# Kernel optimization log

Measured on AMD Instinct MI355X. Metric: run time of the kernel, lower is better.

The kernel has to match this reference:

```python
import jax, jax.numpy as jnp
import numpy as np

N_PTS = 32768      # n_x == n_y (query points == source points)
K_NBR = 32         # neighbors per query point
N_EDGES = N_PTS * K_NBR
D_COORD = 3
C = 64             # f_y channels == MLP output channels
H = 256            # MLP hidden width


def setup_inputs() -> dict:
    key = jax.random.key(0)
    ks = jax.random.split(key, 12)
    y = jax.random.normal(ks[0], (N_PTS, D_COORD), dtype=jnp.float32)
    x = jax.random.normal(ks[1], (N_PTS, D_COORD), dtype=jnp.float32)
    f_y = jax.random.normal(ks[2], (N_PTS, C), dtype=jnp.float32)
    neighbors_index = jax.random.randint(ks[3], (N_EDGES,), 0, N_PTS, dtype=jnp.int64)
    neighbors_row_splits = (jnp.arange(N_PTS + 1, dtype=jnp.int64) * K_NBR)
    weights = jax.random.uniform(ks[4], (N_EDGES,), dtype=jnp.float32)
    # LinearChannelMLP params: layers [6, 256, 256, 64], gelu between layers
    def dense(k, fan_in, fan_out):
        w = jax.random.normal(k, (fan_in, fan_out), dtype=jnp.float32) / np.sqrt(fan_in)
        return w
    W0 = dense(ks[5], 2 * D_COORD, H)
    b0 = jnp.zeros((H,), dtype=jnp.float32)
    W1 = dense(ks[6], H, H)
    b1 = jnp.zeros((H,), dtype=jnp.float32)
    W2 = dense(ks[7], H, C)
    b2 = jnp.zeros((C,), dtype=jnp.float32)
    return {"y": y, "x": x, "f_y": f_y,
            "neighbors_index": neighbors_index,
            "neighbors_row_splits": neighbors_row_splits,
            "weights": weights,
            "W0": W0, "b0": b0, "W1": W1, "b1": b1, "W2": W2, "b2": b2}


def reference(y, x, f_y, neighbors_index, neighbors_row_splits, weights,
              W0, b0, W1, b1, W2, b2):
    n_x = neighbors_row_splits.shape[0] - 1
    n_edges = neighbors_index.shape[0]
    # CSR row id for each edge (equivalent to repeat(arange(n_x), num_reps))
    seg = jnp.searchsorted(neighbors_row_splits, jnp.arange(n_edges), side='right') - 1
    rep_features = y[neighbors_index]            # [E, 3] gathered source coords
    self_features = x[seg]                       # [E, 3] repeated query coords
    agg = jnp.concatenate([rep_features, self_features], axis=-1)  # [E, 6]
    # channel MLP (gelu between layers, none after last)
    h = jax.nn.gelu(agg @ W0 + b0)
    h = jax.nn.gelu(h @ W1 + b1)
    rep = h @ W2 + b2                            # [E, C] kernel values
    # transform_type='linear': kernel * f_y(neighbor)
    rep = rep * f_y[neighbors_index]
    # quadrature weights (forces sum reduction, as in source)
    rep = rep * weights[:, None]
    out = jax.ops.segment_sum(rep, seg, num_segments=n_x)  # segment-CSR sum
    return out
```

## Files before the change

### kernel.cpp

```cpp
#include <hip/hip_runtime.h>
#include <hip/hip_bf16.h>
#include <stdint.h>

#define NPTS 32768
#define KNBR 32
#define NEDGES (NPTS * KNBR)
#define TM 128
#define AGG_STRIDE 40
#define H_STRIDE 264

typedef __attribute__((ext_vector_type(8))) short short8;
typedef __attribute__((ext_vector_type(4))) float f32x4;
typedef __attribute__((ext_vector_type(4))) unsigned int u32x4;
typedef __attribute__((ext_vector_type(2))) unsigned int u32x2;

__device__ __forceinline__ unsigned short f2bf(float f) {
    unsigned int u = __float_as_uint(f);
    unsigned int r = (u + 0x7FFFu + ((u >> 16) & 1u)) >> 16;
    return (unsigned short)r;
}

__device__ __forceinline__ unsigned int cvt_pk_bf16(float lo, float hi) {
    unsigned int r;
    asm("v_cvt_pk_bf16_f32 %0, %1, %2" : "=v"(r) : "v"(lo), "v"(hi));
    return r;
}

__device__ __forceinline__ float gelu_tanh(float x) {
    float x2 = x * x;
    float u = fmaf(-0.102942496f, x2, -2.30220824f);
    float e = __builtin_amdgcn_exp2f(x * u);
    return x * __builtin_amdgcn_rcpf(1.0f + e);
}

__global__ void pack_w(const float* __restrict__ W0, const float* __restrict__ W1,
                       const float* __restrict__ W2, unsigned short* __restrict__ wp) {
    int tid = blockIdx.x * blockDim.x + threadIdx.x;
    if (tid >= 176 * 64) return;
    int fid = tid >> 6, l = tid & 63, ln = l & 15, lg = l >> 4;
    unsigned short v[8];
    if (fid < 16) {
        int nt = fid, k0 = lg * 8;
        #pragma unroll
        for (int j = 0; j < 8; ++j) {
            int k = k0 + j;
            v[j] = f2bf(k < 6 ? W0[k * 256 + nt * 16 + ln] : 0.0f);
        }
    } else if (fid < 144) {
        int g = fid - 16;
        int nt = g >> 3, s = g & 7;
        int col = nt * 16 + ln;
        int k0 = s * 32 + lg * 8;
        #pragma unroll
        for (int j = 0; j < 8; ++j) v[j] = f2bf(W1[(k0 + j) * 256 + col]);
    } else {
        int g = fid - 144;
        int c = g >> 3, s = g & 7;
        int col = c * 16 + ln;
        int k0 = s * 32 + lg * 8;
        #pragma unroll
        for (int j = 0; j < 8; ++j) v[j] = f2bf(W2[(k0 + j) * 64 + col]);
    }
    unsigned short* o = &wp[tid * 8];
    #pragma unroll
    for (int j = 0; j < 8; ++j) o[j] = v[j];
}

__global__ __launch_bounds__(512, 4)
void gno_fused(const float* __restrict__ y, const float* __restrict__ x,
               const float* __restrict__ f_y, const int* __restrict__ nbr,
               const float* __restrict__ wts,
               const float* __restrict__ b0, const float* __restrict__ b1,
               const float* __restrict__ b2,
               const unsigned short* __restrict__ wp,
               float* __restrict__ out) {
    __shared__ __align__(16) unsigned short agg_lds[TM * AGG_STRIDE];
    __shared__ __align__(16) unsigned short h_lds[TM * H_STRIDE];

    const int b = blockIdx.x;
    const int tid = threadIdx.x;
    const int l = tid & 63;
    const int w = tid >> 6;
    const int wm = w & 1;
    const int wn = w >> 1;
    const int lg = l >> 4;
    const int ln = l & 15;
    const int ebase = b * TM;

    const char* wpb = (const char*)wp;
    const char* pW0 = wpb + wn * 4096 + l * 16;
    const char* pW1 = wpb + 16384 + wn * 32768 + l * 16;
    const char* pW2 = wpb + 147456 + wn * 8192 + l * 16;
    const char* aggb = (const char*)agg_lds + ln * 80 + lg * 16;
    char* hwb = (char*)h_lds + ln * 528 + wn * 128 + lg * 8;
    const char* hrb = (const char*)h_lds + ln * 528 + lg * 16;

    if (tid < TM) {
        int e = ebase + tid;
        int j = nbr[e];
        int i = e >> 5;
        const float* yr = &y[j * 3];
        const float* xr = &x[i * 3];
        u32x4 q0;
        q0.x = cvt_pk_bf16(yr[0], yr[1]);
        q0.y = cvt_pk_bf16(yr[2], xr[0]);
        q0.z = cvt_pk_bf16(xr[1], xr[2]);
        q0.w = 0u;
        u32x4 z = {0u, 0u, 0u, 0u};
        unsigned short* row = &agg_lds[tid * AGG_STRIDE];
        *(u32x4*)(row +  0) = q0;
        *(u32x4*)(row +  8) = z;
        *(u32x4*)(row + 16) = z;
        *(u32x4*)(row + 24) = z;
    }
    __syncthreads();

    {
        short8 ag[4];
        #pragma unroll
        for (int mt = 0; mt < 4; ++mt)
            ag[mt] = *(const short8*)(aggb + (4 * wm + mt) * 1280);
        #pragma unroll
        for (int q = 0; q < 4; ++q) {
            short8 aw = *(const short8*)(pW0 + q * 1024);
            f32x4 b0f = *(const f32x4*)&b0[(4 * wn + q) * 16 + lg * 4];
            #pragma unroll
            for (int mt = 0; mt < 4; ++mt) {
                f32x4 c = __builtin_amdgcn_mfma_f32_16x16x32_bf16(aw, ag[mt], b0f, 0, 0, 0);
                u32x2 pv;
                pv.x = cvt_pk_bf16(gelu_tanh(c[0]), gelu_tanh(c[1]));
                pv.y = cvt_pk_bf16(gelu_tanh(c[2]), gelu_tanh(c[3]));
                *(u32x2*)(hwb + (4 * wm + mt) * 8448 + q * 32) = pv;
            }
        }
    }
    __syncthreads();

    f32x4 acc[4][4];
    #pragma unroll
    for (int q = 0; q < 4; ++q) {
        f32x4 b1f = *(const f32x4*)&b1[(4 * wn + q) * 16 + lg * 4];
        #pragma unroll
        for (int mt = 0; mt < 4; ++mt) acc[mt][q] = b1f;
    }
    #pragma unroll
    for (int s = 0; s < 8; ++s) {
        short8 hb[4];
        #pragma unroll
        for (int mt = 0; mt < 4; ++mt)
            hb[mt] = *(const short8*)(hrb + (4 * wm + mt) * 8448 + s * 64);
        #pragma unroll
        for (int q = 0; q < 4; ++q) {
            short8 aw = *(const short8*)(pW1 + q * 8192 + s * 1024);
            #pragma unroll
            for (int mt = 0; mt < 4; ++mt)
                acc[mt][q] = __builtin_amdgcn_mfma_f32_16x16x32_bf16(aw, hb[mt], acc[mt][q], 0, 0, 0);
        }
    }
    __syncthreads();

    #pragma unroll
    for (int q = 0; q < 4; ++q) {
        #pragma unroll
        for (int mt = 0; mt < 4; ++mt) {
            u32x2 pv;
            pv.x = cvt_pk_bf16(gelu_tanh(acc[mt][q][0]), gelu_tanh(acc[mt][q][1]));
            pv.y = cvt_pk_bf16(gelu_tanh(acc[mt][q][2]), gelu_tanh(acc[mt][q][3]));
            *(u32x2*)(hwb + (4 * wm + mt) * 8448 + q * 32) = pv;
        }
    }
    __syncthreads();

    f32x4 fy[4];
    float wv[4];
    #pragma unroll
    for (int m = 0; m < 4; ++m) {
        int e = ebase + (wm * 4 + m) * 16 + ln;
        int j = nbr[e];
        fy[m] = *(const f32x4*)&f_y[j * 64 + wn * 16 + lg * 4];
        wv[m] = wts[e];
    }

    f32x4 acc3[4];
    {
        f32x4 b2f = *(const f32x4*)&b2[wn * 16 + lg * 4];
        #pragma unroll
        for (int m = 0; m < 4; ++m) acc3[m] = b2f;
    }
    const char* hrb3 = hrb + wm * 33792;
    #pragma unroll
    for (int s = 0; s < 8; ++s) {
        short8 aw = *(const short8*)(pW2 + s * 1024);
        #pragma unroll
        for (int m = 0; m < 4; ++m) {
            short8 hb = *(const short8*)(hrb3 + m * 8448 + s * 64);
            acc3[m] = __builtin_amdgcn_mfma_f32_16x16x32_bf16(aw, hb, acc3[m], 0, 0, 0);
        }
    }

    {
        f32x4 seg[2];
        seg[0] = (f32x4){0.f, 0.f, 0.f, 0.f};
        seg[1] = (f32x4){0.f, 0.f, 0.f, 0.f};
        #pragma unroll
        for (int m = 0; m < 4; ++m) {
            f32x4 v;
            #pragma unroll
            for (int i = 0; i < 4; ++i)
                v[i] = acc3[m][i] * fy[m][i] * wv[m];
            seg[m >> 1] += v;
        }
        #pragma unroll
        for (int g = 0; g < 2; ++g) {
            f32x4 v = seg[g];
            #pragma unroll
            for (int d = 1; d <= 8; d <<= 1) {
                #pragma unroll
                for (int i = 0; i < 4; ++i)
                    v[i] += __shfl_xor(v[i], d, 64);
            }
            if (ln == 0)
                *(f32x4*)&out[(b * 4 + wm * 2 + g) * 64 + wn * 16 + lg * 4] = v;
        }
    }
}

extern "C" void kernel_launch(void* const* d_in, const int* in_sizes, int n_in,
                              void* d_out, int out_size, void* d_ws, size_t ws_size,
                              hipStream_t stream) {
    const float* y   = (const float*)d_in[0];
    const float* x   = (const float*)d_in[1];
    const float* f_y = (const float*)d_in[2];
    const int*   nbr = (const int*)d_in[3];
    const float* wts = (const float*)d_in[5];
    const float* W0  = (const float*)d_in[6];
    const float* b0  = (const float*)d_in[7];
    const float* W1  = (const float*)d_in[8];
    const float* b1  = (const float*)d_in[9];
    const float* W2  = (const float*)d_in[10];
    const float* b2  = (const float*)d_in[11];
    unsigned short* wp = (unsigned short*)d_ws;
    float* out = (float*)d_out;

    pack_w<<<dim3(44), dim3(256), 0, stream>>>(W0, W1, W2, wp);
    gno_fused<<<dim3(NEDGES / TM), dim3(512), 0, stream>>>(
        y, x, f_y, nbr, wts, b0, b1, b2, wp, out);
}
```

Measured before the change: 278.9 us.

## Halve edge tile to 64 per block and raise occupancy target

Reduces the per-block edge tile from 128 to 64 rows, so each wave handles two M-tiles instead of four. Accumulator register and LDS footprint per block drop, and the launch bound is raised to allow six blocks per CU. Two inner loops become partially unrolled. In exchange, the packed weights are re-read from global/L2 twice as often per edge, and there are twice as many blocks and barriers.

```diff
diff --git a/kernel.cpp b/kernel.cpp
--- a/kernel.cpp
+++ b/kernel.cpp
@@ -5,7 +5,7 @@
 #define NPTS 32768
 #define KNBR 32
 #define NEDGES (NPTS * KNBR)
-#define TM 128
+#define TM 64
 #define AGG_STRIDE 40
 #define H_STRIDE 264
 
@@ -66,7 +66,7 @@
     for (int j = 0; j < 8; ++j) o[j] = v[j];
 }
 
-__global__ __launch_bounds__(512, 4)
+__global__ __launch_bounds__(512, 6)
 void gno_fused(const float* __restrict__ y, const float* __restrict__ x,
                const float* __restrict__ f_y, const int* __restrict__ nbr,
                const float* __restrict__ wts,
@@ -116,45 +116,41 @@
     __syncthreads();
 
     {
-        short8 ag[4];
-        #pragma unroll
-        for (int mt = 0; mt < 4; ++mt)
-            ag[mt] = *(const short8*)(aggb + (4 * wm + mt) * 1280);
+        short8 ag0 = *(const short8*)(aggb + (2 * wm + 0) * 1280);
+        short8 ag1 = *(const short8*)(aggb + (2 * wm + 1) * 1280);
         #pragma unroll
         for (int q = 0; q < 4; ++q) {
             short8 aw = *(const short8*)(pW0 + q * 1024);
             f32x4 b0f = *(const f32x4*)&b0[(4 * wn + q) * 16 + lg * 4];
-            #pragma unroll
-            for (int mt = 0; mt < 4; ++mt) {
-                f32x4 c = __builtin_amdgcn_mfma_f32_16x16x32_bf16(aw, ag[mt], b0f, 0, 0, 0);
-                u32x2 pv;
-                pv.x = cvt_pk_bf16(gelu_tanh(c[0]), gelu_tanh(c[1]));
-                pv.y = cvt_pk_bf16(gelu_tanh(c[2]), gelu_tanh(c[3]));
-                *(u32x2*)(hwb + (4 * wm + mt) * 8448 + q * 32) = pv;
-            }
-        }
-    }
-    __syncthreads();
-
-    f32x4 acc[4][4];
+            f32x4 c0 = __builtin_amdgcn_mfma_f32_16x16x32_bf16(aw, ag0, b0f, 0, 0, 0);
+            f32x4 c1 = __builtin_amdgcn_mfma_f32_16x16x32_bf16(aw, ag1, b0f, 0, 0, 0);
+            u32x2 p0, p1;
+            p0.x = cvt_pk_bf16(gelu_tanh(c0[0]), gelu_tanh(c0[1]));
+            p0.y = cvt_pk_bf16(gelu_tanh(c0[2]), gelu_tanh(c0[3]));
+            p1.x = cvt_pk_bf16(gelu_tanh(c1[0]), gelu_tanh(c1[1]));
+            p1.y = cvt_pk_bf16(gelu_tanh(c1[2]), gelu_tanh(c1[3]));
+            *(u32x2*)(hwb + (2 * wm + 0) * 8448 + q * 32) = p0;
+            *(u32x2*)(hwb + (2 * wm + 1) * 8448 + q * 32) = p1;
+        }
+    }
+    __syncthreads();
+
+    f32x4 acc[2][4];
     #pragma unroll
     for (int q = 0; q < 4; ++q) {
         f32x4 b1f = *(const f32x4*)&b1[(4 * wn + q) * 16 + lg * 4];
-        #pragma unroll
-        for (int mt = 0; mt < 4; ++mt) acc[mt][q] = b1f;
-    }
-    #pragma unroll
+        acc[0][q] = b1f;
+        acc[1][q] = b1f;
+    }
+    #pragma unroll 2
     for (int s = 0; s < 8; ++s) {
-        short8 hb[4];
-        #pragma unroll
-        for (int mt = 0; mt < 4; ++mt)
-            hb[mt] = *(const short8*)(hrb + (4 * wm + mt) * 8448 + s * 64);
+        short8 hb0 = *(const short8*)(hrb + (2 * wm + 0) * 8448 + s * 64);
+        short8 hb1 = *(const short8*)(hrb + (2 * wm + 1) * 8448 + s * 64);
         #pragma unroll
         for (int q = 0; q < 4; ++q) {
             short8 aw = *(const short8*)(pW1 + q * 8192 + s * 1024);
-            #pragma unroll
-            for (int mt = 0; mt < 4; ++mt)
-                acc[mt][q] = __builtin_amdgcn_mfma_f32_16x16x32_bf16(aw, hb[mt], acc[mt][q], 0, 0, 0);
+            acc[0][q] = __builtin_amdgcn_mfma_f32_16x16x32_bf16(aw, hb0, acc[0][q], 0, 0, 0);
+            acc[1][q] = __builtin_amdgcn_mfma_f32_16x16x32_bf16(aw, hb1, acc[1][q], 0, 0, 0);
         }
     }
     __syncthreads();
@@ -162,66 +158,56 @@
     #pragma unroll
     for (int q = 0; q < 4; ++q) {
         #pragma unroll
-        for (int mt = 0; mt < 4; ++mt) {
+        for (int m = 0; m < 2; ++m) {
             u32x2 pv;
-            pv.x = cvt_pk_bf16(gelu_tanh(acc[mt][q][0]), gelu_tanh(acc[mt][q][1]));
-            pv.y = cvt_pk_bf16(gelu_tanh(acc[mt][q][2]), gelu_tanh(acc[mt][q][3]));
-            *(u32x2*)(hwb + (4 * wm + mt) * 8448 + q * 32) = pv;
-        }
-    }
-    __syncthreads();
-
-    f32x4 fy[4];
-    float wv[4];
-    #pragma unroll
-    for (int m = 0; m < 4; ++m) {
-        int e = ebase + (wm * 4 + m) * 16 + ln;
+            pv.x = cvt_pk_bf16(gelu_tanh(acc[m][q][0]), gelu_tanh(acc[m][q][1]));
+            pv.y = cvt_pk_bf16(gelu_tanh(acc[m][q][2]), gelu_tanh(acc[m][q][3]));
+            *(u32x2*)(hwb + (2 * wm + m) * 8448 + q * 32) = pv;
+        }
+    }
+    __syncthreads();
+
+    f32x4 fy[2];
+    float wv[2];
+    #pragma unroll
+    for (int m = 0; m < 2; ++m) {
+        int e = ebase + (2 * wm + m) * 16 + ln;
         int j = nbr[e];
         fy[m] = *(const f32x4*)&f_y[j * 64 + wn * 16 + lg * 4];
         wv[m] = wts[e];
     }
 
-    f32x4 acc3[4];
+    f32x4 acc3[2];
     {
         f32x4 b2f = *(const f32x4*)&b2[wn * 16 + lg * 4];
-        #pragma unroll
-        for (int m = 0; m < 4; ++m) acc3[m] = b2f;
-    }
-    const char* hrb3 = hrb + wm * 33792;
-    #pragma unroll
+        acc3[0] = b2f;
+        acc3[1] = b2f;
+    }
+    #pragma unroll 2
     for (int s = 0; s < 8; ++s) {
         short8 aw = *(const short8*)(pW2 + s * 1024);
-        #pragma unroll
-        for (int m = 0; m < 4; ++m) {
-            short8 hb = *(const short8*)(hrb3 + m * 8448 + s * 64);
-            acc3[m] = __builtin_amdgcn_mfma_f32_16x16x32_bf16(aw, hb, acc3[m], 0, 0, 0);
-        }
+        short8 hb0 = *(const short8*)(hrb + (2 * wm + 0) * 8448 + s * 64);
+        short8 hb1 = *(const short8*)(hrb + (2 * wm + 1) * 8448 + s * 64);
+        acc3[0] = __builtin_amdgcn_mfma_f32_16x16x32_bf16(aw, hb0, acc3[0], 0, 0, 0);
+        acc3[1] = __builtin_amdgcn_mfma_f32_16x16x32_bf16(aw, hb1, acc3[1], 0, 0, 0);
     }
 
     {
-        f32x4 seg[2];
-        seg[0] = (f32x4){0.f, 0.f, 0.f, 0.f};
-        seg[1] = (f32x4){0.f, 0.f, 0.f, 0.f};
-        #pragma unroll
-        for (int m = 0; m < 4; ++m) {
-            f32x4 v;
+        f32x4 seg = {0.f, 0.f, 0.f, 0.f};
+        #pragma unroll
+        for (int m = 0; m < 2; ++m) {
             #pragma unroll
             for (int i = 0; i < 4; ++i)
-                v[i] = acc3[m][i] * fy[m][i] * wv[m];
-            seg[m >> 1] += v;
-        }
-        #pragma unroll
-        for (int g = 0; g < 2; ++g) {
-            f32x4 v = seg[g];
+                seg[i] += acc3[m][i] * fy[m][i] * wv[m];
+        }
+        #pragma unroll
+        for (int d = 1; d <= 8; d <<= 1) {
             #pragma unroll
-            for (int d = 1; d <= 8; d <<= 1) {
-                #pragma unroll
-                for (int i = 0; i < 4; ++i)
-                    v[i] += __shfl_xor(v[i], d, 64);
-            }
-            if (ln == 0)
-                *(f32x4*)&out[(b * 4 + wm * 2 + g) * 64 + wn * 16 + lg * 4] = v;
-        }
+            for (int i = 0; i < 4; ++i)
+                seg[i] += __shfl_xor(seg[i], d, 64);
+        }
+        if (ln == 0)
+            *(f32x4*)&out[(2 * b + wm) * 64 + wn * 16 + lg * 4] = seg;
     }
 }
 
```

Measured after the change: 306.6 us. 9.9% more time.
